# Kernel optimization log

Measured on AMD Instinct MI355X. Metric: run time of the kernel, lower is better.

Reference implementation:

```python
import jax, jax.numpy as jnp
import numpy as np

N_USERS = 8192
N_ITEMS = 4096
BATCH = 8192


def setup_inputs() -> dict:
    key = jax.random.key(0)
    k1, k2, k3, k4, k5, k6, k7 = jax.random.split(key, 7)
    # ratings in {0..5}; zeros mark unrated entries (needed for nonzero masking)
    rating_mtx = jax.random.randint(k1, (N_USERS, N_ITEMS), 0, 6).astype(jnp.float32)
    user = jax.random.randint(k2, (BATCH,), 0, N_USERS)
    item = jax.random.randint(k3, (BATCH,), 0, N_ITEMS)
    # learned parameters (xavier-normal similarity; biases initialized like global mean)
    xavier_std = float(np.sqrt(2.0 / (N_USERS + N_USERS)))
    user_similarity = jax.random.normal(k4, (N_USERS, N_USERS), dtype=jnp.float32) * xavier_std
    user_bias = jax.random.normal(k5, (N_USERS,), dtype=jnp.float32)
    item_bias = jax.random.normal(k6, (N_ITEMS,), dtype=jnp.float32)
    global_bias = jax.random.normal(k7, (), dtype=jnp.float32)
    return {
        "user": user,
        "item": item,
        "rating_mtx": rating_mtx,
        "user_similarity": user_similarity,
        "user_bias": user_bias,
        "item_bias": item_bias,
        "global_bias": global_bias,
    }


def reference(user, item, rating_mtx, user_similarity, user_bias, item_bias, global_bias):
    # per-user mean over NONZERO ratings (0 if user rated nothing) -- single fused
    # masked sum/count reduction replacing the per-row python loop
    mask = rating_mtx != 0  # [U, I]
    cnt = jnp.sum(mask, axis=1)  # [U]
    row_sum = jnp.sum(rating_mtx, axis=1)  # zeros contribute nothing
    user_bias_fixed = jnp.where(cnt > 0, row_sum / jnp.maximum(cnt, 1).astype(rating_mtx.dtype), 0.0)

    adjusted = rating_mtx - user_bias_fixed[:, None]  # [U, I]
    similarities = user_similarity[user]  # [B, U]
    item_ratings = adjusted[:, item]  # [U, B]
    user_scores = jnp.sum(similarities * item_ratings.T, axis=1)  # [B]

    bias = user_bias[user] + item_bias[item] + global_bias  # [B]
    return jax.nn.sigmoid(user_scores + bias) * 5.0
```

## Files before the change

### kernel.cpp

```cpp
#include <hip/hip_runtime.h>
#include <math.h>

#define N_USERS 8192
#define N_ITEMS 4096
#define BATCH   8192

__global__ __launch_bounds__(256) void k_ubfix(const float* __restrict__ R,
                                               float* __restrict__ ub) {
    const int u = blockIdx.x;
    const float4* row4 = (const float4*)(R + (size_t)u * N_ITEMS);
    float s = 0.f, c = 0.f;
    for (int i = threadIdx.x; i < N_ITEMS / 4; i += 256) {
        float4 v = row4[i];
        s += v.x + v.y + v.z + v.w;
        c += (v.x != 0.f) + (v.y != 0.f) + (v.z != 0.f) + (v.w != 0.f);
    }
    for (int off = 32; off; off >>= 1) {
        s += __shfl_down(s, off);
        c += __shfl_down(c, off);
    }
    __shared__ float sa[4], sc[4];
    const int lane = threadIdx.x & 63, w = threadIdx.x >> 6;
    if (lane == 0) { sa[w] = s; sc[w] = c; }
    __syncthreads();
    if (threadIdx.x == 0) {
        float rs = sa[0] + sa[1] + sa[2] + sa[3];
        float cnt = sc[0] + sc[1] + sc[2] + sc[3];
        ub[u] = (cnt > 0.f) ? rs / fmaxf(cnt, 1.f) : 0.f;
    }
}

__global__ __launch_bounds__(256) void k_transpose(const float* __restrict__ R,
                                                   const float* __restrict__ ub,
                                                   float* __restrict__ AT) {
    __shared__ float lds[64][65];
    const int colBase = blockIdx.x * 64;
    const int rowBase = blockIdx.y * 64;
    const int tx = threadIdx.x, ty = threadIdx.y;
    const int x4 = tx * 4;

    #pragma unroll
    for (int k = 0; k < 4; ++k) {
        const int y = ty + 16 * k;
        float4 v = *(const float4*)(R + (size_t)(rowBase + y) * N_ITEMS + colBase + x4);
        lds[y][x4 + 0] = v.x;
        lds[y][x4 + 1] = v.y;
        lds[y][x4 + 2] = v.z;
        lds[y][x4 + 3] = v.w;
    }
    __syncthreads();

    const float u0 = ub[rowBase + x4 + 0];
    const float u1 = ub[rowBase + x4 + 1];
    const float u2 = ub[rowBase + x4 + 2];
    const float u3 = ub[rowBase + x4 + 3];

    #pragma unroll
    for (int k = 0; k < 4; ++k) {
        const int y = ty + 16 * k;
        float4 w;
        w.x = lds[x4 + 0][y] - u0;
        w.y = lds[x4 + 1][y] - u1;
        w.z = lds[x4 + 2][y] - u2;
        w.w = lds[x4 + 3][y] - u3;
        *(float4*)(AT + (size_t)(colBase + y) * N_USERS + rowBase + x4) = w;
    }
}

__global__ __launch_bounds__(256) void k_main(const float* __restrict__ S,
                                              const float* __restrict__ AT,
                                              const int* __restrict__ user,
                                              const int* __restrict__ item,
                                              const float* __restrict__ ubias,
                                              const float* __restrict__ ibias,
                                              const float* __restrict__ gbias,
                                              float* __restrict__ out) {
    const int b = blockIdx.x;
    const int su = user[b];
    const int j  = item[b];
    const float4* srow = (const float4*)(S  + (size_t)su * N_USERS);
    const float4* arow = (const float4*)(AT + (size_t)j  * N_USERS);
    float acc = 0.f;
    for (int i = threadIdx.x; i < N_USERS / 4; i += 256) {
        float4 a = srow[i];
        float4 r = arow[i];
        acc += a.x * r.x + a.y * r.y + a.z * r.z + a.w * r.w;
    }
    for (int off = 32; off; off >>= 1) acc += __shfl_down(acc, off);
    __shared__ float sa[4];
    const int lane = threadIdx.x & 63, w = threadIdx.x >> 6;
    if (lane == 0) sa[w] = acc;
    __syncthreads();
    if (threadIdx.x == 0) {
        float score = sa[0] + sa[1] + sa[2] + sa[3]
                    + ubias[su] + ibias[j] + gbias[0];
        out[b] = 5.f / (1.f + expf(-score));
    }
}

__global__ __launch_bounds__(256) void k_direct(const float* __restrict__ S,
                                                const float* __restrict__ R,
                                                const float* __restrict__ ub,
                                                const int* __restrict__ user,
                                                const int* __restrict__ item,
                                                const float* __restrict__ ubias,
                                                const float* __restrict__ ibias,
                                                const float* __restrict__ gbias,
                                                float* __restrict__ out) {
    const int b = blockIdx.x;
    const int su = user[b];
    const int j  = item[b];
    const float* srow = S + (size_t)su * N_USERS;
    float acc = 0.f;
    for (int u = threadIdx.x; u < N_USERS; u += 256) {
        acc += srow[u] * (R[(size_t)u * N_ITEMS + j] - ub[u]);
    }
    for (int off = 32; off; off >>= 1) acc += __shfl_down(acc, off);
    __shared__ float sa[4];
    const int lane = threadIdx.x & 63, w = threadIdx.x >> 6;
    if (lane == 0) sa[w] = acc;
    __syncthreads();
    if (threadIdx.x == 0) {
        float score = sa[0] + sa[1] + sa[2] + sa[3]
                    + ubias[su] + ibias[j] + gbias[0];
        out[b] = 5.f / (1.f + expf(-score));
    }
}

extern "C" void kernel_launch(void* const* d_in, const int* in_sizes, int n_in,
                              void* d_out, int out_size, void* d_ws, size_t ws_size,
                              hipStream_t stream) {
    const int*   user  = (const int*)d_in[0];
    const int*   item  = (const int*)d_in[1];
    const float* R     = (const float*)d_in[2];
    const float* S     = (const float*)d_in[3];
    const float* ubias = (const float*)d_in[4];
    const float* ibias = (const float*)d_in[5];
    const float* gbias = (const float*)d_in[6];
    float* out = (float*)d_out;

    float* ub = (float*)d_ws;
    float* AT = (float*)((char*)d_ws + 65536);
    const size_t need = 65536 + (size_t)N_ITEMS * N_USERS * sizeof(float);

    k_ubfix<<<N_USERS, 256, 0, stream>>>(R, ub);

    if (ws_size >= need) {
        dim3 tgrid(N_ITEMS / 64, N_USERS / 64);
        dim3 tblk(16, 16);
        k_transpose<<<tgrid, tblk, 0, stream>>>(R, ub, AT);
        k_main<<<BATCH, 256, 0, stream>>>(S, AT, user, item, ubias, ibias, gbias, out);
    } else {
        k_direct<<<BATCH, 256, 0, stream>>>(S, R, ub, user, item, ubias, ibias, gbias, out);
    }
}
```

Before: 492.5 us.

## Store adjusted rating transpose in bf16 and use one wave per row

The transposed, bias-adjusted rating matrix is now written as bf16 with round-to-nearest-even instead of fp32. This halves the transpose's write traffic and the AT bytes k_main reads per batch row. Both k_ubfix and k_main now assign one 64-lane wave per row or batch element, which removes the LDS cross-wave reduction and __syncthreads. The cost is reduced precision in the adjusted ratings that feed the dot product.

```diff
diff --git a/kernel.cpp b/kernel.cpp
--- a/kernel.cpp
+++ b/kernel.cpp
@@ -5,34 +5,44 @@
 #define N_ITEMS 4096
 #define BATCH   8192
 
+__device__ __forceinline__ unsigned short f32_to_bf16_rne(float f) {
+    union { float f; unsigned int u; } cvt;
+    cvt.f = f;
+    unsigned int u = cvt.u;
+    u += 0x7fffu + ((u >> 16) & 1u);
+    return (unsigned short)(u >> 16);
+}
+__device__ __forceinline__ float bf16_bits_to_f32(unsigned int h) {
+    union { unsigned int u; float f; } cvt;
+    cvt.u = h << 16;
+    return cvt.f;
+}
+
 __global__ __launch_bounds__(256) void k_ubfix(const float* __restrict__ R,
                                                float* __restrict__ ub) {
-    const int u = blockIdx.x;
+    const int wave = threadIdx.x >> 6;
+    const int lane = threadIdx.x & 63;
+    const int u = blockIdx.x * 4 + wave;
     const float4* row4 = (const float4*)(R + (size_t)u * N_ITEMS);
     float s = 0.f, c = 0.f;
-    for (int i = threadIdx.x; i < N_ITEMS / 4; i += 256) {
-        float4 v = row4[i];
+    #pragma unroll
+    for (int i = 0; i < 16; ++i) {
+        float4 v = row4[i * 64 + lane];
         s += v.x + v.y + v.z + v.w;
         c += (v.x != 0.f) + (v.y != 0.f) + (v.z != 0.f) + (v.w != 0.f);
     }
+    #pragma unroll
     for (int off = 32; off; off >>= 1) {
         s += __shfl_down(s, off);
         c += __shfl_down(c, off);
     }
-    __shared__ float sa[4], sc[4];
-    const int lane = threadIdx.x & 63, w = threadIdx.x >> 6;
-    if (lane == 0) { sa[w] = s; sc[w] = c; }
-    __syncthreads();
-    if (threadIdx.x == 0) {
-        float rs = sa[0] + sa[1] + sa[2] + sa[3];
-        float cnt = sc[0] + sc[1] + sc[2] + sc[3];
-        ub[u] = (cnt > 0.f) ? rs / fmaxf(cnt, 1.f) : 0.f;
-    }
+    if (lane == 0)
+        ub[u] = (c > 0.f) ? s / fmaxf(c, 1.f) : 0.f;
 }
 
 __global__ __launch_bounds__(256) void k_transpose(const float* __restrict__ R,
                                                    const float* __restrict__ ub,
-                                                   float* __restrict__ AT) {
+                                                   unsigned short* __restrict__ AT) {
     __shared__ float lds[64][65];
     const int colBase = blockIdx.x * 64;
     const int rowBase = blockIdx.y * 64;
@@ -58,42 +68,52 @@
     #pragma unroll
     for (int k = 0; k < 4; ++k) {
         const int y = ty + 16 * k;
-        float4 w;
-        w.x = lds[x4 + 0][y] - u0;
-        w.y = lds[x4 + 1][y] - u1;
-        w.z = lds[x4 + 2][y] - u2;
-        w.w = lds[x4 + 3][y] - u3;
-        *(float4*)(AT + (size_t)(colBase + y) * N_USERS + rowBase + x4) = w;
+        ushort4 w;
+        w.x = f32_to_bf16_rne(lds[x4 + 0][y] - u0);
+        w.y = f32_to_bf16_rne(lds[x4 + 1][y] - u1);
+        w.z = f32_to_bf16_rne(lds[x4 + 2][y] - u2);
+        w.w = f32_to_bf16_rne(lds[x4 + 3][y] - u3);
+        *(ushort4*)(AT + (size_t)(colBase + y) * N_USERS + rowBase + x4) = w;
     }
 }
 
 __global__ __launch_bounds__(256) void k_main(const float* __restrict__ S,
-                                              const float* __restrict__ AT,
+                                              const unsigned short* __restrict__ AT,
                                               const int* __restrict__ user,
                                               const int* __restrict__ item,
                                               const float* __restrict__ ubias,
                                               const float* __restrict__ ibias,
                                               const float* __restrict__ gbias,
                                               float* __restrict__ out) {
-    const int b = blockIdx.x;
+    const int wave = threadIdx.x >> 6;
+    const int lane = threadIdx.x & 63;
+    const int b = blockIdx.x * 4 + wave;
     const int su = user[b];
     const int j  = item[b];
-    const float4* srow = (const float4*)(S  + (size_t)su * N_USERS);
-    const float4* arow = (const float4*)(AT + (size_t)j  * N_USERS);
+    const float4* srow = (const float4*)(S + (size_t)su * N_USERS);
+    const uint4*  arow = (const uint4*)(AT + (size_t)j * N_USERS);
+
     float acc = 0.f;
-    for (int i = threadIdx.x; i < N_USERS / 4; i += 256) {
-        float4 a = srow[i];
-        float4 r = arow[i];
-        acc += a.x * r.x + a.y * r.y + a.z * r.z + a.w * r.w;
+    #pragma unroll 4
+    for (int i = 0; i < 16; ++i) {
+        const int idx = i * 64 + lane;
+        uint4  a  = arow[idx];
+        float4 s0 = srow[idx * 2 + 0];
+        float4 s1 = srow[idx * 2 + 1];
+        acc += s0.x * bf16_bits_to_f32(a.x & 0xffffu);
+        acc += s0.y * bf16_bits_to_f32(a.x >> 16);
+        acc += s0.z * bf16_bits_to_f32(a.y & 0xffffu);
+        acc += s0.w * bf16_bits_to_f32(a.y >> 16);
+        acc += s1.x * bf16_bits_to_f32(a.z & 0xffffu);
+        acc += s1.y * bf16_bits_to_f32(a.z >> 16);
+        acc += s1.z * bf16_bits_to_f32(a.w & 0xffffu);
+        acc += s1.w * bf16_bits_to_f32(a.w >> 16);
     }
+    #pragma unroll
     for (int off = 32; off; off >>= 1) acc += __shfl_down(acc, off);
-    __shared__ float sa[4];
-    const int lane = threadIdx.x & 63, w = threadIdx.x >> 6;
-    if (lane == 0) sa[w] = acc;
-    __syncthreads();
-    if (threadIdx.x == 0) {
-        float score = sa[0] + sa[1] + sa[2] + sa[3]
-                    + ubias[su] + ibias[j] + gbias[0];
+
+    if (lane == 0) {
+        float score = acc + ubias[su] + ibias[j] + gbias[0];
         out[b] = 5.f / (1.f + expf(-score));
     }
 }
@@ -140,16 +160,16 @@
     float* out = (float*)d_out;
 
     float* ub = (float*)d_ws;
-    float* AT = (float*)((char*)d_ws + 65536);
-    const size_t need = 65536 + (size_t)N_ITEMS * N_USERS * sizeof(float);
+    unsigned short* AT = (unsigned short*)((char*)d_ws + 65536);
+    const size_t need = 65536 + (size_t)N_ITEMS * N_USERS * sizeof(unsigned short);
 
-    k_ubfix<<<N_USERS, 256, 0, stream>>>(R, ub);
+    k_ubfix<<<N_USERS / 4, 256, 0, stream>>>(R, ub);
 
     if (ws_size >= need) {
         dim3 tgrid(N_ITEMS / 64, N_USERS / 64);
         dim3 tblk(16, 16);
         k_transpose<<<tgrid, tblk, 0, stream>>>(R, ub, AT);
-        k_main<<<BATCH, 256, 0, stream>>>(S, AT, user, item, ubias, ibias, gbias, out);
+        k_main<<<BATCH / 4, 256, 0, stream>>>(S, AT, user, item, ubias, ibias, gbias, out);
     } else {
         k_direct<<<BATCH, 256, 0, stream>>>(S, R, ub, user, item, ubias, ibias, gbias, out);
     }
```

Result: faster. 470.8 us (-4.4%).
